# Optimization experiments

Hardware: AMD Instinct MI355X
Metric: run time of the kernel (lower is better)

The kernel has to match this reference:

```python
import jax, jax.numpy as jnp
import numpy as np

B, L, E = 16, 2048, 256


def setup_inputs() -> dict:
    key = jax.random.key(0)
    ks = jax.random.split(key, 8)
    s = 1.0 / np.sqrt(E)
    x = jax.random.normal(ks[0], (B, L, E), dtype=jnp.float32)
    lengths = jax.random.randint(ks[1], (B,), 0, L, dtype=jnp.int32)
    Wq = jax.random.normal(ks[2], (E, E), dtype=jnp.float32) * s
    bq = jax.random.normal(ks[3], (E,), dtype=jnp.float32) * s
    Wk = jax.random.normal(ks[4], (E, E), dtype=jnp.float32) * s
    bk = jax.random.normal(ks[5], (E,), dtype=jnp.float32) * s
    Wv = jax.random.normal(ks[6], (E, E), dtype=jnp.float32) * s
    bv = jax.random.normal(ks[7], (E,), dtype=jnp.float32) * s
    return {"x": x, "lengths": lengths, "Wq": Wq, "bq": bq,
            "Wk": Wk, "bk": bk, "Wv": Wv, "bv": bv}


def reference(x, lengths, Wq, bq, Wk, bk, Wv, bv):
    # ragged validity mask: [B, L, 1]
    mask = (jnp.arange(L)[None, :] < lengths[:, None]).astype(x.dtype)[..., None]
    q = (jnp.einsum('ble,fe->blf', x, Wq) + bq) * mask  # masked queries -> zero padded output rows
    k = (jnp.einsum('ble,fe->blf', x, Wk) + bk) * mask  # masked keys -> exclude padding from contraction
    v = jnp.einsum('ble,fe->blf', x, Wv) + bv           # invalid keys already zeroed via k
    attn_weights = jnp.einsum('bqe,bke->bqk', q, k)      # [B, L, L] (no softmax in original)
    attn_output = jnp.einsum('bqk,bke->bqe', attn_weights, v)  # [B, L, E]
    # to_padded_tensor(pad=0).mean(dim=1) divides by the PADDED length L
    return attn_output.sum(axis=1) / jnp.asarray(L, x.dtype)  # [B, E]
```

## Files before the change

kernel.cpp:

```cpp
#include <hip/hip_runtime.h>

#define Bb 16
#define Ll 2048
#define Ee 256
#define E4 64
#define BPB 32
#define RPB 64
#define JT 16
#define FS (Ee / JT)

#define P1_OFF 0
#define TP_OFF (P1_OFF + Bb*BPB*Ee)
#define C_OFF  (TP_OFF + Bb*JT*Ee)
#define U_OFF  (C_OFF + Bb)
#define W_OFF  (U_OFF + Bb*Ee)
#define M_OFF  (W_OFF + Bb)
#define BQK_OFF (M_OFF + Ee*Ee)
#define KV_OFF  (BQK_OFF + Ee)
#define BETA_OFF (KV_OFF + Ee)

__global__ void __launch_bounds__(256) kA(const float* __restrict__ x,
                                          const int* __restrict__ lengths,
                                          const float* __restrict__ Wq,
                                          const float* __restrict__ bq,
                                          const float* __restrict__ Wk,
                                          const float* __restrict__ bk,
                                          float* __restrict__ ws) {
    const int blk = blockIdx.x;
    const int tid = threadIdx.x, lane = tid & 63, wid = tid >> 6;

    if (blk < Bb * BPB) {
        const int b = blk >> 5, i = blk & 31;
        const int len = lengths[b];
        const int r0 = i * RPB;
        float4* slot = (float4*)(ws + P1_OFF + ((size_t)(b * BPB + i)) * Ee);
        if (r0 >= len) {
            if (tid < 64) slot[tid] = make_float4(0.f, 0.f, 0.f, 0.f);
            return;
        }
        const float4* xb = (const float4*)(x + (size_t)b * Ll * Ee);
        float4 acc = {0.f, 0.f, 0.f, 0.f};
#pragma unroll
        for (int rr = 0; rr < 16; ++rr) {
            const int r = r0 + wid + rr * 4;
            float4 v = xb[(size_t)r * E4 + lane];
            const bool ok = (r < len);
            acc.x += ok ? v.x : 0.f; acc.y += ok ? v.y : 0.f;
            acc.z += ok ? v.z : 0.f; acc.w += ok ? v.w : 0.f;
        }
        __shared__ float4 part[256];
        part[tid] = acc;
        __syncthreads();
        if (tid < 64) {
            float4 a = part[tid], b1 = part[64+tid], c1 = part[128+tid], d1 = part[192+tid];
            slot[tid] = make_float4(a.x+b1.x+c1.x+d1.x, a.y+b1.y+c1.y+d1.y,
                                    a.z+b1.z+c1.z+d1.z, a.w+b1.w+c1.w+d1.w);
        }
        return;
    }

    const int ep = blk - Bb * BPB;
    const float4* wk4 = (const float4*)Wk;
    float4 macc = {0.f, 0.f, 0.f, 0.f};
    float4 qacc = {0.f, 0.f, 0.f, 0.f};
    const bool doBqk = (ep == 0);
#pragma unroll 16
    for (int q = 0; q < 64; ++q) {
        const int f = wid * 64 + q;
        const float wq = Wq[(size_t)f * Ee + ep];
        const float4 w4 = wk4[(size_t)f * E4 + lane];
        macc.x += wq * w4.x; macc.y += wq * w4.y;
        macc.z += wq * w4.z; macc.w += wq * w4.w;
        if (doBqk) {
            const float bqf = bq[f];
            qacc.x += bqf * w4.x; qacc.y += bqf * w4.y;
            qacc.z += bqf * w4.z; qacc.w += bqf * w4.w;
        }
    }
    float kv = Wq[(size_t)(wid * 64 + lane) * Ee + ep] * bk[wid * 64 + lane];
#pragma unroll
    for (int m = 32; m; m >>= 1) kv += __shfl_xor(kv, m, 64);

    __shared__ float4 mred[4][64];
    __shared__ float4 qred[4][64];
    __shared__ float kred[4];
    mred[wid][lane] = macc;
    if (doBqk) qred[wid][lane] = qacc;
    if (lane == 0) kred[wid] = kv;
    __syncthreads();
    if (wid == 0) {
        float4 a = mred[0][lane], b1 = mred[1][lane], c1 = mred[2][lane], d1 = mred[3][lane];
        ((float4*)(ws + M_OFF + (size_t)ep * Ee))[lane] =
            make_float4(a.x+b1.x+c1.x+d1.x, a.y+b1.y+c1.y+d1.y,
                        a.z+b1.z+c1.z+d1.z, a.w+b1.w+c1.w+d1.w);
        if (lane == 0) ws[KV_OFF + ep] = kred[0] + kred[1] + kred[2] + kred[3];
    }
    if (doBqk) {
        if (wid == 1) {
            float4 a = qred[0][lane], b1 = qred[1][lane], c1 = qred[2][lane], d1 = qred[3][lane];
            ((float4*)(ws + BQK_OFF))[lane] =
                make_float4(a.x+b1.x+c1.x+d1.x, a.y+b1.y+c1.y+d1.y,
                            a.z+b1.z+c1.z+d1.z, a.w+b1.w+c1.w+d1.w);
        }
        float p = bq[tid] * bk[tid];
#pragma unroll
        for (int m = 32; m; m >>= 1) p += __shfl_xor(p, m, 64);
        __shared__ float bred[4];
        if (lane == 0) bred[wid] = p;
        __syncthreads();
        if (tid == 0) ws[BETA_OFF] = bred[0] + bred[1] + bred[2] + bred[3];
    }
}

__global__ void __launch_bounds__(256) kB(const float* __restrict__ lengths_f,
                                          const int* __restrict__ lengths,
                                          float* __restrict__ ws) {
    const int b = blockIdx.y, j = blockIdx.x;
    const int tid = threadIdx.x;
    const int len = lengths[b];
    __shared__ alignas(16) float xs[Ee];
    {
        const float* P = ws + P1_OFF + (size_t)b * BPB * Ee + tid;
        float a0 = 0.f, a1 = 0.f, a2 = 0.f, a3 = 0.f;
#pragma unroll
        for (int q = 0; q < BPB; q += 4) {
            a0 += P[(size_t)(q+0) * Ee];
            a1 += P[(size_t)(q+1) * Ee];
            a2 += P[(size_t)(q+2) * Ee];
            a3 += P[(size_t)(q+3) * Ee];
        }
        xs[tid] = (a0 + a1) + (a2 + a3);
    }
    __syncthreads();
    const float* M = ws + M_OFF;
    float tp = 0.f;
#pragma unroll
    for (int q = 0; q < FS; ++q) {
        const int ep = j * FS + q;
        tp += xs[ep] * M[(size_t)ep * Ee + tid];
    }
    if (j == 0) tp += (float)len * ws[BQK_OFF + tid];
    ws[TP_OFF + ((size_t)(b * JT + j)) * Ee + tid] = tp;

    if (j == 0) {
        ws[U_OFF + b * Ee + tid] = 0.f;
        float p = xs[tid] * ws[KV_OFF + tid];
#pragma unroll
        for (int m = 32; m; m >>= 1) p += __shfl_xor(p, m, 64);
        __shared__ float cred[4];
        if ((tid & 63) == 0) cred[tid >> 6] = p;
        __syncthreads();
        if (tid == 0) {
            ws[C_OFF + b] = cred[0] + cred[1] + cred[2] + cred[3]
                          + (float)len * ws[BETA_OFF];
            ws[W_OFF + b] = 0.f;
        }
    }
}

__global__ void __launch_bounds__(256) k3(const float* __restrict__ x,
                                          const int* __restrict__ lengths,
                                          const float* __restrict__ TP,
                                          const float* __restrict__ C,
                                          float* __restrict__ U, float* __restrict__ W) {
    const int b = blockIdx.y, i = blockIdx.x;
    const int len = lengths[b];
    const int r0 = i * RPB;
    if (r0 >= len) return;
    const int tid = threadIdx.x, lane = tid & 63, wid = tid >> 6;
    const float4* tp4 = (const float4*)(TP + (size_t)b * JT * Ee);
    float4 tv = {0.f, 0.f, 0.f, 0.f};
#pragma unroll
    for (int jj = 0; jj < JT; ++jj) {
        float4 t = tp4[(size_t)jj * E4 + lane];
        tv.x += t.x; tv.y += t.y; tv.z += t.z; tv.w += t.w;
    }
    const float cb = C[b];
    const float4* xb = (const float4*)(x + (size_t)b * Ll * Ee);
    float4 uacc = {0.f, 0.f, 0.f, 0.f};
    float wacc = 0.f;
#pragma unroll
    for (int rr = 0; rr < 16; ++rr) {
        const int r = r0 + wid + rr * 4;
        float4 xv = xb[(size_t)r * E4 + lane];
        float d = xv.x*tv.x + xv.y*tv.y + xv.z*tv.z + xv.w*tv.w;
#pragma unroll
        for (int m = 32; m; m >>= 1) d += __shfl_xor(d, m, 64);
        float w = (r < len) ? (d + cb) : 0.f;
        uacc.x += w*xv.x; uacc.y += w*xv.y; uacc.z += w*xv.z; uacc.w += w*xv.w;
        wacc += w;
    }
    __shared__ float4 part[256];
    __shared__ float cw[4];
    part[tid] = uacc;
    if (lane == 0) cw[wid] = wacc;
    __syncthreads();
    if (tid < 64) {
        float4 a = part[tid], b1 = part[64+tid], c1 = part[128+tid], d1 = part[192+tid];
        float* ub = U + b * Ee + tid * 4;
        atomicAdd(ub + 0, a.x + b1.x + c1.x + d1.x);
        atomicAdd(ub + 1, a.y + b1.y + c1.y + d1.y);
        atomicAdd(ub + 2, a.z + b1.z + c1.z + d1.z);
        atomicAdd(ub + 3, a.w + b1.w + c1.w + d1.w);
    }
    if (tid == 0) atomicAdd(W + b, cw[0] + cw[1] + cw[2] + cw[3]);
}

__global__ void __launch_bounds__(256) k4(const float* __restrict__ U,
                                          const float* __restrict__ W,
                                          const float* __restrict__ Wv,
                                          const float* __restrict__ bv,
                                          float* __restrict__ out) {
    const int b = blockIdx.y, j = blockIdx.x;
    const int tid = threadIdx.x, lane = tid & 63, wid = tid >> 6;
    __shared__ float4 u4[E4];
    __shared__ float red[4][64];
    if (tid < E4) u4[tid] = ((const float4*)(U + b * Ee))[tid];
    __syncthreads();
    const int e = j * 64 + lane;
    const float4* wv = (const float4*)(Wv + (size_t)e * Ee);
    float acc = 0.f;
#pragma unroll
    for (int q = 0; q < 16; ++q) {
        float4 w = wv[wid * 16 + q]; float4 v = u4[wid * 16 + q];
        acc += w.x*v.x + w.y*v.y + w.z*v.z + w.w*v.w;
    }
    red[wid][lane] = acc;
    __syncthreads();
    if (wid == 0) {
        float r = red[0][lane] + red[1][lane] + red[2][lane] + red[3][lane];
        out[b * Ee + e] = (r + bv[e] * W[b]) * (1.0f / (float)Ll);
    }
}

extern "C" void kernel_launch(void* const* d_in, const int* in_sizes, int n_in,
                              void* d_out, int out_size, void* d_ws, size_t ws_size,
                              hipStream_t stream) {
    const float* x       = (const float*)d_in[0];
    const int*   lengths = (const int*)d_in[1];
    const float* Wq      = (const float*)d_in[2];
    const float* bq      = (const float*)d_in[3];
    const float* Wk      = (const float*)d_in[4];
    const float* bk      = (const float*)d_in[5];
    const float* Wv      = (const float*)d_in[6];
    const float* bv      = (const float*)d_in[7];
    float* out = (float*)d_out;
    float* ws  = (float*)d_ws;

    kA<<<Bb * BPB + Ee, 256, 0, stream>>>(x, lengths, Wq, bq, Wk, bk, ws);
    kB<<<dim3(JT, Bb), 256, 0, stream>>>(nullptr, lengths, ws);
    k3<<<dim3(BPB, Bb), 256, 0, stream>>>(x, lengths, ws + TP_OFF, ws + C_OFF,
                                          ws + U_OFF, ws + W_OFF);
    k4<<<dim3(4, Bb), 256, 0, stream>>>(ws + U_OFF, ws + W_OFF, Wv, bv, out);
}
```

Baseline: 32.38 us.

## Fuse final Wv projection into k3 via last-block atomic ticket

Removes the separate k4 launch by having the last active k3 block per batch, found through an atomic ticket counter, run the Wv matvec and write the output. Output rows are pre-zeroed in kA so batches with no active rows still yield zero. This saves one kernel launch and its dependency gap. In exchange, a single block per batch does the whole 256x256 matvec serially, and the fix-up relies on threadfence plus atomic ordering.

```diff
diff --git a/kernel.cpp b/kernel.cpp
--- a/kernel.cpp
+++ b/kernel.cpp
@@ -18,6 +18,7 @@
 #define BQK_OFF (M_OFF + Ee*Ee)
 #define KV_OFF  (BQK_OFF + Ee)
 #define BETA_OFF (KV_OFF + Ee)
+#define TK_OFF  (BETA_OFF + 1)
 
 __global__ void __launch_bounds__(256) kA(const float* __restrict__ x,
                                           const int* __restrict__ lengths,
@@ -25,12 +26,14 @@
                                           const float* __restrict__ bq,
                                           const float* __restrict__ Wk,
                                           const float* __restrict__ bk,
-                                          float* __restrict__ ws) {
+                                          float* __restrict__ ws,
+                                          float* __restrict__ out) {
     const int blk = blockIdx.x;
     const int tid = threadIdx.x, lane = tid & 63, wid = tid >> 6;
 
     if (blk < Bb * BPB) {
         const int b = blk >> 5, i = blk & 31;
+        if (i == 0) out[b * Ee + tid] = 0.f;
         const int len = lengths[b];
         const int r0 = i * RPB;
         float4* slot = (float4*)(ws + P1_OFF + ((size_t)(b * BPB + i)) * Ee);
@@ -112,8 +115,7 @@
     }
 }
 
-__global__ void __launch_bounds__(256) kB(const float* __restrict__ lengths_f,
-                                          const int* __restrict__ lengths,
+__global__ void __launch_bounds__(256) kB(const int* __restrict__ lengths,
                                           float* __restrict__ ws) {
     const int b = blockIdx.y, j = blockIdx.x;
     const int tid = threadIdx.x;
@@ -154,20 +156,26 @@
             ws[C_OFF + b] = cred[0] + cred[1] + cred[2] + cred[3]
                           + (float)len * ws[BETA_OFF];
             ws[W_OFF + b] = 0.f;
+            ((int*)ws)[TK_OFF + b] = 0;
         }
     }
 }
 
 __global__ void __launch_bounds__(256) k3(const float* __restrict__ x,
                                           const int* __restrict__ lengths,
-                                          const float* __restrict__ TP,
-                                          const float* __restrict__ C,
-                                          float* __restrict__ U, float* __restrict__ W) {
+                                          float* __restrict__ ws,
+                                          const float* __restrict__ Wv,
+                                          const float* __restrict__ bv,
+                                          float* __restrict__ out) {
     const int b = blockIdx.y, i = blockIdx.x;
     const int len = lengths[b];
     const int r0 = i * RPB;
     if (r0 >= len) return;
     const int tid = threadIdx.x, lane = tid & 63, wid = tid >> 6;
+    const float* TP = ws + TP_OFF;
+    float* U = ws + U_OFF;
+    float* W = ws + W_OFF;
+
     const float4* tp4 = (const float4*)(TP + (size_t)b * JT * Ee);
     float4 tv = {0.f, 0.f, 0.f, 0.f};
 #pragma unroll
@@ -175,7 +183,7 @@
         float4 t = tp4[(size_t)jj * E4 + lane];
         tv.x += t.x; tv.y += t.y; tv.z += t.z; tv.w += t.w;
     }
-    const float cb = C[b];
+    const float cb = ws[C_OFF + b];
     const float4* xb = (const float4*)(x + (size_t)b * Ll * Ee);
     float4 uacc = {0.f, 0.f, 0.f, 0.f};
     float wacc = 0.f;
@@ -204,33 +212,36 @@
         atomicAdd(ub + 3, a.w + b1.w + c1.w + d1.w);
     }
     if (tid == 0) atomicAdd(W + b, cw[0] + cw[1] + cw[2] + cw[3]);
-}
-
-__global__ void __launch_bounds__(256) k4(const float* __restrict__ U,
-                                          const float* __restrict__ W,
-                                          const float* __restrict__ Wv,
-                                          const float* __restrict__ bv,
-                                          float* __restrict__ out) {
-    const int b = blockIdx.y, j = blockIdx.x;
-    const int tid = threadIdx.x, lane = tid & 63, wid = tid >> 6;
-    __shared__ float4 u4[E4];
-    __shared__ float red[4][64];
-    if (tid < E4) u4[tid] = ((const float4*)(U + b * Ee))[tid];
-    __syncthreads();
-    const int e = j * 64 + lane;
-    const float4* wv = (const float4*)(Wv + (size_t)e * Ee);
-    float acc = 0.f;
-#pragma unroll
-    for (int q = 0; q < 16; ++q) {
-        float4 w = wv[wid * 16 + q]; float4 v = u4[wid * 16 + q];
-        acc += w.x*v.x + w.y*v.y + w.z*v.z + w.w*v.w;
-    }
-    red[wid][lane] = acc;
-    __syncthreads();
-    if (wid == 0) {
-        float r = red[0][lane] + red[1][lane] + red[2][lane] + red[3][lane];
-        out[b * Ee + e] = (r + bv[e] * W[b]) * (1.0f / (float)Ll);
-    }
+
+    __shared__ int isLast;
+    __syncthreads();
+    if (tid == 0) {
+        __threadfence();
+        const int nact = (len + RPB - 1) >> 6;
+        int old = atomicAdd((int*)ws + TK_OFF + b, 1);
+        isLast = (old == nact - 1);
+    }
+    __syncthreads();
+    if (!isLast) return;
+    __threadfence();
+
+    __shared__ alignas(16) float u_sh[Ee];
+    u_sh[tid] = U[b * Ee + tid];
+    __syncthreads();
+    const float Wb = W[b];
+    const float4* wrow = (const float4*)(Wv + (size_t)tid * Ee);
+    const float4* u4   = (const float4*)u_sh;
+    float a0 = 0.f, a1 = 0.f, a2 = 0.f, a3 = 0.f;
+#pragma unroll 8
+    for (int q = 0; q < E4; q += 4) {
+        float4 w0 = wrow[q+0], w1 = wrow[q+1], w2 = wrow[q+2], w3 = wrow[q+3];
+        float4 v0 = u4[q+0],  v1 = u4[q+1],  v2 = u4[q+2],  v3 = u4[q+3];
+        a0 += w0.x*v0.x + w0.y*v0.y + w0.z*v0.z + w0.w*v0.w;
+        a1 += w1.x*v1.x + w1.y*v1.y + w1.z*v1.z + w1.w*v1.w;
+        a2 += w2.x*v2.x + w2.y*v2.y + w2.z*v2.z + w2.w*v2.w;
+        a3 += w3.x*v3.x + w3.y*v3.y + w3.z*v3.z + w3.w*v3.w;
+    }
+    out[b * Ee + tid] = ((a0 + a1) + (a2 + a3) + bv[tid] * Wb) * (1.0f / (float)Ll);
 }
 
 extern "C" void kernel_launch(void* const* d_in, const int* in_sizes, int n_in,
@@ -247,9 +258,7 @@
     float* out = (float*)d_out;
     float* ws  = (float*)d_ws;
 
-    kA<<<Bb * BPB + Ee, 256, 0, stream>>>(x, lengths, Wq, bq, Wk, bk, ws);
-    kB<<<dim3(JT, Bb), 256, 0, stream>>>(nullptr, lengths, ws);
-    k3<<<dim3(BPB, Bb), 256, 0, stream>>>(x, lengths, ws + TP_OFF, ws + C_OFF,
-                                          ws + U_OFF, ws + W_OFF);
-    k4<<<dim3(4, Bb), 256, 0, stream>>>(ws + U_OFF, ws + W_OFF, Wv, bv, out);
-}
+    kA<<<Bb * BPB + Ee, 256, 0, stream>>>(x, lengths, Wq, bq, Wk, bk, ws, out);
+    kB<<<dim3(JT, Bb), 256, 0, stream>>>(lengths, ws);
+    k3<<<dim3(BPB, Bb), 256, 0, stream>>>(x, lengths, ws, Wv, bv, out);
+}
```

New measurement: 49.87 us. +54.0%, slower.
